# Optimization experiments

Measured on AMD Instinct MI355X. Metric: run time of the kernel, lower is better.

The kernel has to match this reference:

```python
import jax, jax.numpy as jnp
import numpy as np

N = 65536          # total detections
PER = 64           # boxes per frame (max_per_img)
B = N // PER       # frames
NUM_CLASSES = 36   # len(obj_classes), incl. background
OBJ_DIM = 192
EMB = 200
POS = 128
HID = 1024
EPS = 1e-5


def setup_inputs() -> dict:
    key = jax.random.key(0)
    ks = jax.random.split(key, 16)
    # distribution: per-box class scores over 35 foreground classes
    distribution = jax.random.uniform(ks[0], (N, NUM_CLASSES - 1), jnp.float32)
    features = jax.random.normal(ks[1], (N, OBJ_DIM), jnp.float32)
    # boxes: [img_idx, x1, y1, x2, y2], 64 boxes per frame, img_idx sorted
    img_idx = (jnp.arange(N) // PER).astype(jnp.float32)
    xy1 = jax.random.uniform(ks[2], (N, 2), jnp.float32) * 500.0
    wh = jax.random.uniform(ks[3], (N, 2), jnp.float32) * 100.0 + 1.0
    boxes = jnp.concatenate([img_idx[:, None], xy1, xy1 + wh], axis=1)
    # parameters
    obj_embed_W = jax.random.normal(ks[4], (NUM_CLASSES - 1, EMB), jnp.float32) * 0.1
    bn4_g = jnp.ones((4,), jnp.float32)
    bn4_b = jnp.zeros((4,), jnp.float32)
    bn4_m = jnp.zeros((4,), jnp.float32)
    bn4_v = jnp.ones((4,), jnp.float32)
    pos_W = jax.random.normal(ks[5], (4, POS), jnp.float32) * 0.05
    pos_b = jnp.zeros((POS,), jnp.float32)
    dec1_W = jax.random.normal(ks[6], (OBJ_DIM + EMB + POS, HID), jnp.float32) * 0.02
    dec1_b = jnp.zeros((HID,), jnp.float32)
    bn1k_g = jnp.ones((HID,), jnp.float32)
    bn1k_b = jnp.zeros((HID,), jnp.float32)
    bn1k_m = jnp.zeros((HID,), jnp.float32)
    bn1k_v = jnp.ones((HID,), jnp.float32)
    dec2_W = jax.random.normal(ks[7], (HID, NUM_CLASSES), jnp.float32) * 0.02
    dec2_b = jnp.zeros((NUM_CLASSES,), jnp.float32)
    return dict(distribution=distribution, features=features, boxes=boxes,
                obj_embed_W=obj_embed_W, bn4_g=bn4_g, bn4_b=bn4_b, bn4_m=bn4_m, bn4_v=bn4_v,
                pos_W=pos_W, pos_b=pos_b, dec1_W=dec1_W, dec1_b=dec1_b,
                bn1k_g=bn1k_g, bn1k_b=bn1k_b, bn1k_m=bn1k_m, bn1k_v=bn1k_v,
                dec2_W=dec2_W, dec2_b=dec2_b)


def reference(distribution, features, boxes, obj_embed_W, bn4_g, bn4_b, bn4_m, bn4_v,
              pos_W, pos_b, dec1_W, dec1_b, bn1k_g, bn1k_b, bn1k_m, bn1k_v,
              dec2_W, dec2_b):
    # soft object-class embedding: [N,35] @ [35,200]
    obj_embed = distribution @ obj_embed_W
    # center_size(boxes[:,1:]): (cx, cy, w, h)
    xy1 = boxes[:, 1:3]
    xy2 = boxes[:, 3:5]
    wh = xy2 - xy1 + 1.0
    cs = jnp.concatenate([xy1 + 0.5 * wh, wh], axis=1)
    # pos_embed: BatchNorm1d(4) (eval) -> Linear(4,128) -> ReLU (dropout=id in eval)
    h = (cs - bn4_m) * jax.lax.rsqrt(bn4_v + EPS) * bn4_g + bn4_b
    pos = jax.nn.relu(h @ pos_W + pos_b)
    # decoder_lin: Linear(520,1024) -> BN(1024, eval) -> ReLU -> Linear(1024,36)
    obj_feat = jnp.concatenate([features, obj_embed, pos], axis=1)  # [N,520]
    g = obj_feat @ dec1_W + dec1_b
    g = (g - bn1k_m) * jax.lax.rsqrt(bn1k_v + EPS) * bn1k_g + bn1k_b
    g = jax.nn.relu(g)
    logits = g @ dec2_W + dec2_b  # [N,36]
    # drop background, softmax over foreground classes
    dist = jax.nn.softmax(logits[:, 1:], axis=1)  # [N,35]
    pred_scores = jnp.max(dist[:, 1:], axis=1)
    pred_labels = jnp.argmax(dist[:, 1:], axis=1) + 2
    # per-frame human argmax over class-0 (human) score; 64 boxes per frame
    human_local = jnp.argmax(dist[:, 0].reshape(B, PER), axis=1)
    human_idx = jnp.arange(B) * PER + human_local  # [B]
    pred_labels = pred_labels.at[human_idx].set(1)
    pred_scores = pred_scores.at[human_idx].set(dist[human_idx, 0])
    return dist, pred_scores, pred_labels, human_idx
```

## Files before the change

### kernel.cpp

```cpp
#include <hip/hip_runtime.h>
#include <math.h>

#define NROWS 65536
#define PER 64
#define BIMG 1024
#define NCLS 36
#define OBJ_DIM 192
#define EMB 200
#define POSD 128
#define HID 1024
#define EPSV 1e-5f

#define KP 384
#define XSTR 392
#define LSTR 52


typedef __attribute__((ext_vector_type(8))) _Float16 f16x8;
typedef __attribute__((ext_vector_type(4))) _Float16 f16x4;
typedef __attribute__((ext_vector_type(4))) float f32x4;

__global__ __launch_bounds__(256) void k_fold(
    const float* __restrict__ obj_embed_W, const float* __restrict__ dec1_W,
    float* __restrict__ Fold)
{
    int e = blockIdx.x;
    int h = blockIdx.y * 256 + threadIdx.x;
    const float* A  = obj_embed_W + (size_t)e * EMB;
    const float* Bp = dec1_W + (size_t)192 * HID + h;
    float acc = 0.f;
#pragma unroll 8
    for (int j = 0; j < EMB; ++j)
        acc = fmaf(A[j], Bp[(size_t)j * HID], acc);
    Fold[(size_t)e * HID + h] = acc;
}

__global__ __launch_bounds__(256) void k_prep(
    const float* __restrict__ Fold, const float* __restrict__ dec1_W,
    const float* __restrict__ dec1_b,
    const float* __restrict__ bn1k_g, const float* __restrict__ bn1k_b,
    const float* __restrict__ bn1k_m, const float* __restrict__ bn1k_v,
    const float* __restrict__ dec2_W,
    _Float16* __restrict__ W1p, _Float16* __restrict__ W2p,
    float* __restrict__ bs)
{
    int idx = blockIdx.x * 256 + threadIdx.x;
    if (idx < HID * KP) {
        int e  = idx & 7;
        int l  = (idx >> 3) & 63;
        int ks = (idx >> 9) % 12;
        int ht = idx / 6144;
        int h = ht * 16 + (l & 15);
        int k = ks * 32 + (l >> 4) * 8 + e;
        float sc = rsqrtf(bn1k_v[h] + EPSV) * bn1k_g[h];
        float v;
        if (k < 192)      v = dec1_W[(size_t)k * HID + h];
        else if (k < 320) v = dec1_W[(size_t)(k + 200) * HID + h];
        else if (k < 355) v = Fold[(size_t)(k - 320) * HID + h];
        else              v = 0.f;
        W1p[idx] = (_Float16)(v * sc);
        if (k == 0) bs[h] = (dec1_b[h] - bn1k_m[h]) * sc + bn1k_b[h];
    } else {
        int p2 = idx - HID * KP;
        if (p2 < 64 * 3 * 256) {
            int e   = p2 & 3;
            int l   = (p2 >> 2) & 63;
            int cls = (p2 >> 8) % 3;
            int ht  = p2 / 768;
            int h = 16 * ht + 4 * (l >> 4) + e;
            int c = 16 * cls + (l & 15);
            W2p[p2] = (c < NCLS) ? (_Float16)dec2_W[(size_t)h * NCLS + c] : (_Float16)0.f;
        }
    }
}

__global__ __launch_bounds__(256, 2) void k_main(
    const float* __restrict__ distribution, const float* __restrict__ features,
    const float* __restrict__ boxes,
    const float* __restrict__ bn4_g, const float* __restrict__ bn4_b,
    const float* __restrict__ bn4_m, const float* __restrict__ bn4_v,
    const float* __restrict__ pos_W, const float* __restrict__ pos_b,
    const _Float16* __restrict__ W1p, const _Float16* __restrict__ W2p,
    const float* __restrict__ bs, const float* __restrict__ dec2_b,
    float* __restrict__ out)
{
    __shared__ __align__(16) char smem[53248];
    _Float16* Xs = (_Float16*)smem;
    float* Lst   = (float*)smem;

    int t = threadIdx.x;
    int row0 = blockIdx.x * PER;
    int wv = t >> 6, lane = t & 63, lr = lane & 15, lq = lane >> 4;

    {
        const f32x4* F4 = (const f32x4*)(features + (size_t)row0 * OBJ_DIM);
#pragma unroll
        for (int it = 0; it < 12; ++it) {
            int li = t + 256 * it;
            int r = li / 48, c4 = li % 48;
            f32x4 v = __builtin_nontemporal_load(F4 + li);
            f16x4 h4;
            h4[0] = (_Float16)v[0]; h4[1] = (_Float16)v[1];
            h4[2] = (_Float16)v[2]; h4[3] = (_Float16)v[3];
            *(f16x4*)&Xs[r * XSTR + c4 * 4] = h4;
        }
        const float* D = distribution + (size_t)row0 * (NCLS - 1);
#pragma unroll
        for (int it = 0; it < 2; ++it) {
            int li = t + 256 * it;
            int r = li >> 3, gq = li & 7;
            f16x8 v8;
#pragma unroll
            for (int e = 0; e < 8; ++e) {
                int c = gq * 8 + e;
                v8[e] = (c < 35) ? (_Float16)__builtin_nontemporal_load(D + (size_t)r * 35 + c)
                                 : (_Float16)0.f;
            }
            *(f16x8*)&Xs[r * XSTR + 320 + gq * 8] = v8;
        }
        int r = t >> 2, kq = t & 3;
        int grow = row0 + r;
        const float* bx = boxes + (size_t)grow * 5;
        float x1 = bx[1], y1 = bx[2], x2 = bx[3], y2 = bx[4];
        float w = x2 - x1 + 1.f, hh = y2 - y1 + 1.f;
        float cs[4] = {x1 + 0.5f * w, y1 + 0.5f * hh, w, hh};
        float hv[4];
#pragma unroll
        for (int i = 0; i < 4; i++)
            hv[i] = (cs[i] - bn4_m[i]) * rsqrtf(bn4_v[i] + EPSV) * bn4_g[i] + bn4_b[i];
#pragma unroll
        for (int jb = 0; jb < 4; ++jb) {
            int j0 = kq * 32 + jb * 8;
            f16x8 v8;
#pragma unroll
            for (int e = 0; e < 8; ++e) {
                int j = j0 + e;
                float p = pos_b[j];
                p = fmaf(hv[0], pos_W[j], p);
                p = fmaf(hv[1], pos_W[POSD + j], p);
                p = fmaf(hv[2], pos_W[2 * POSD + j], p);
                p = fmaf(hv[3], pos_W[3 * POSD + j], p);
                v8[e] = (_Float16)fmaxf(p, 0.f);
            }
            *(f16x8*)&Xs[r * XSTR + 192 + j0] = v8;
        }
    }
    __syncthreads();

    f32x4 Lg[4][3];
#pragma unroll
    for (int n = 0; n < 4; n++)
#pragma unroll
        for (int cls = 0; cls < 3; cls++) Lg[n][cls] = (f32x4){0.f, 0.f, 0.f, 0.f};

    for (int c0 = 0; c0 < 4; ++c0) {
        const _Float16* ap = W1p + ((size_t)(16 * c0 + wv) * 12) * 512 + (size_t)lane * 8;

        f32x4 C[4][4];
#pragma unroll
        for (int j = 0; j < 4; j++)
#pragma unroll
            for (int n = 0; n < 4; n++) C[j][n] = (f32x4){0.f, 0.f, 0.f, 0.f};

#pragma unroll 4
        for (int ks = 0; ks < 12; ++ks) {
            f16x8 ah[4], bh[4];
#pragma unroll
            for (int j = 0; j < 4; j++)
                ah[j] = *(const f16x8*)(ap + ((size_t)(4 * j) * 12 + ks) * 512);
#pragma unroll
            for (int n = 0; n < 4; n++)
                bh[n] = *(const f16x8*)&Xs[(16 * n + lr) * XSTR + ks * 32 + lq * 8];
#pragma unroll
            for (int j = 0; j < 4; j++)
#pragma unroll
                for (int n = 0; n < 4; n++)
                    C[j][n] = __builtin_amdgcn_mfma_f32_16x16x32_f16(ah[j], bh[n], C[j][n], 0, 0, 0);
        }

#pragma unroll
        for (int j = 0; j < 4; ++j) {
            int ht = 16 * c0 + wv + 4 * j;
            f32x4 bsv = *(const f32x4*)(bs + 16 * ht + 4 * lq);
            f16x4 af[4];
#pragma unroll
            for (int n = 0; n < 4; n++)
#pragma unroll
                for (int e = 0; e < 4; ++e)
                    af[n][e] = (_Float16)fmaxf(C[j][n][e] + bsv[e], 0.f);
#pragma unroll
            for (int cls = 0; cls < 3; ++cls) {
                f16x4 bf = *(const f16x4*)(W2p + ((size_t)(ht * 3 + cls) * 64 + lane) * 4);
#pragma unroll
                for (int n = 0; n < 4; n++)
                    Lg[n][cls] = __builtin_amdgcn_mfma_f32_16x16x16f16(af[n], bf, Lg[n][cls], 0, 0, 0);
            }
        }
    }

    __syncthreads();
    {
        float* Lw = Lst + (size_t)wv * 64 * LSTR;
#pragma unroll
        for (int n = 0; n < 4; n++)
#pragma unroll
            for (int cls = 0; cls < 3; cls++)
#pragma unroll
                for (int e = 0; e < 4; ++e)
                    Lw[(16 * n + 4 * lq + e) * LSTR + 16 * cls + lr] = Lg[n][cls][e];
    }
    __syncthreads();

    if (t < 64) {
        int row = row0 + t;
        float lg[36];
#pragma unroll
        for (int c = 1; c < 36; ++c)
            lg[c] = Lst[t * LSTR + c] + Lst[64 * LSTR + t * LSTR + c]
                  + Lst[128 * LSTR + t * LSTR + c] + Lst[192 * LSTR + t * LSTR + c]
                  + dec2_b[c];
        float m = lg[1];
#pragma unroll
        for (int c = 2; c < 36; ++c) m = fmaxf(m, lg[c]);
        float d[35];
        float s = 0.f;
#pragma unroll
        for (int c = 1; c < 36; ++c) { float e = expf(lg[c] - m); d[c - 1] = e; s += e; }
        float inv = 1.0f / s;
        float* dout = out + (size_t)row * 35;
#pragma unroll
        for (int j = 0; j < 35; ++j) dout[j] = d[j] * inv;

        float best = -1.f; int bi = 1;
#pragma unroll
        for (int c = 1; c < 35; ++c) {
            float v = d[c] * inv;
            if (v > best) { best = v; bi = c; }
        }

        float v0 = d[0] * inv;
        float mv = v0; int mi = t;
#pragma unroll
        for (int off = 32; off > 0; off >>= 1) {
            float ov = __shfl_down(mv, off);
            int   oi = __shfl_down(mi, off);
            if (ov > mv || (ov == mv && oi < mi)) { mv = ov; mi = oi; }
        }
        int human = __shfl(mi, 0);
        bool isH = (t == human);
        out[(size_t)NROWS * 35 + row] = isH ? v0 : best;
        out[(size_t)NROWS * 36 + row] = isH ? 1.0f : (float)(bi + 1);
        if (t == 0) out[(size_t)NROWS * 37 + blockIdx.x] = (float)(row0 + human);
    }
}

extern "C" void kernel_launch(void* const* d_in, const int* in_sizes, int n_in,
                              void* d_out, int out_size, void* d_ws, size_t ws_size,
                              hipStream_t stream)
{
    (void)in_sizes; (void)n_in; (void)out_size; (void)ws_size;
    const float* distribution = (const float*)d_in[0];
    const float* features     = (const float*)d_in[1];
    const float* boxes        = (const float*)d_in[2];
    const float* obj_embed_W  = (const float*)d_in[3];
    const float* bn4_g        = (const float*)d_in[4];
    const float* bn4_b        = (const float*)d_in[5];
    const float* bn4_m        = (const float*)d_in[6];
    const float* bn4_v        = (const float*)d_in[7];
    const float* pos_W        = (const float*)d_in[8];
    const float* pos_b        = (const float*)d_in[9];
    const float* dec1_W       = (const float*)d_in[10];
    const float* dec1_b       = (const float*)d_in[11];
    const float* bn1k_g       = (const float*)d_in[12];
    const float* bn1k_b       = (const float*)d_in[13];
    const float* bn1k_m       = (const float*)d_in[14];
    const float* bn1k_v       = (const float*)d_in[15];
    const float* dec2_W       = (const float*)d_in[16];
    const float* dec2_b       = (const float*)d_in[17];

    float* out = (float*)d_out;

    _Float16* W1p  = (_Float16*)d_ws;
    _Float16* W2p  = W1p + (size_t)HID * KP;
    float*    bsv  = (float*)(W2p + (size_t)64 * 3 * 256);
    float*    Fold = bsv + HID;

    k_fold<<<dim3(35, 4), 256, 0, stream>>>(obj_embed_W, dec1_W, Fold);

    int prep_elems = HID * KP + 64 * 3 * 256;
    k_prep<<<(prep_elems + 255) / 256, 256, 0, stream>>>(
        Fold, dec1_W, dec1_b, bn1k_g, bn1k_b, bn1k_m, bn1k_v, dec2_W,
        W1p, W2p, bsv);

    k_main<<<BIMG, 256, 0, stream>>>(
        distribution, features, boxes, bn4_g, bn4_b, bn4_m, bn4_v, pos_W, pos_b,
        W1p, W2p, bsv, dec2_b, out);
}
```

Baseline: 226.7 us.

## Process two frames per 512-thread block so wave groups share W1 slices

Each block now handles 128 rows (two frames) with 8 waves. Two groups of four waves read the same W1 tiles, each against its own 64-row half of the shared activation buffer, so weight fetches can be reused through cache. Shared memory doubles to about 104 KB and the grid halves. The ks loop unroll drops from 4 to 2. The larger LDS footprint likely limits each CU to one block, and the coarser grid may worsen tail imbalance across CUs.

```diff
diff --git a/kernel.cpp b/kernel.cpp
--- a/kernel.cpp
+++ b/kernel.cpp
@@ -4,6 +4,7 @@
 #define NROWS 65536
 #define PER 64
 #define BIMG 1024
+#define NBLK 512
 #define NCLS 36
 #define OBJ_DIM 192
 #define EMB 200
@@ -74,7 +75,7 @@
     }
 }
 
-__global__ __launch_bounds__(256, 2) void k_main(
+__global__ __launch_bounds__(512, 2) void k_main(
     const float* __restrict__ distribution, const float* __restrict__ features,
     const float* __restrict__ boxes,
     const float* __restrict__ bn4_g, const float* __restrict__ bn4_b,
@@ -84,19 +85,20 @@
     const float* __restrict__ bs, const float* __restrict__ dec2_b,
     float* __restrict__ out)
 {
-    __shared__ __align__(16) char smem[53248];
+    __shared__ __align__(16) char smem[106496];
     _Float16* Xs = (_Float16*)smem;
     float* Lst   = (float*)smem;
 
     int t = threadIdx.x;
-    int row0 = blockIdx.x * PER;
+    int row0 = blockIdx.x * 128;
     int wv = t >> 6, lane = t & 63, lr = lane & 15, lq = lane >> 4;
+    int s = wv & 3, g = wv >> 2;
 
     {
         const f32x4* F4 = (const f32x4*)(features + (size_t)row0 * OBJ_DIM);
 #pragma unroll
         for (int it = 0; it < 12; ++it) {
-            int li = t + 256 * it;
+            int li = t + 512 * it;
             int r = li / 48, c4 = li % 48;
             f32x4 v = __builtin_nontemporal_load(F4 + li);
             f16x4 h4;
@@ -107,7 +109,7 @@
         const float* D = distribution + (size_t)row0 * (NCLS - 1);
 #pragma unroll
         for (int it = 0; it < 2; ++it) {
-            int li = t + 256 * it;
+            int li = t + 512 * it;
             int r = li >> 3, gq = li & 7;
             f16x8 v8;
 #pragma unroll
@@ -154,7 +156,7 @@
         for (int cls = 0; cls < 3; cls++) Lg[n][cls] = (f32x4){0.f, 0.f, 0.f, 0.f};
 
     for (int c0 = 0; c0 < 4; ++c0) {
-        const _Float16* ap = W1p + ((size_t)(16 * c0 + wv) * 12) * 512 + (size_t)lane * 8;
+        const _Float16* ap = W1p + ((size_t)(16 * c0 + s) * 12) * 512 + (size_t)lane * 8;
 
         f32x4 C[4][4];
 #pragma unroll
@@ -162,7 +164,7 @@
 #pragma unroll
             for (int n = 0; n < 4; n++) C[j][n] = (f32x4){0.f, 0.f, 0.f, 0.f};
 
-#pragma unroll 4
+#pragma unroll 2
         for (int ks = 0; ks < 12; ++ks) {
             f16x8 ah[4], bh[4];
 #pragma unroll
@@ -170,7 +172,7 @@
                 ah[j] = *(const f16x8*)(ap + ((size_t)(4 * j) * 12 + ks) * 512);
 #pragma unroll
             for (int n = 0; n < 4; n++)
-                bh[n] = *(const f16x8*)&Xs[(16 * n + lr) * XSTR + ks * 32 + lq * 8];
+                bh[n] = *(const f16x8*)&Xs[(64 * g + 16 * n + lr) * XSTR + ks * 32 + lq * 8];
 #pragma unroll
             for (int j = 0; j < 4; j++)
 #pragma unroll
@@ -180,7 +182,7 @@
 
 #pragma unroll
         for (int j = 0; j < 4; ++j) {
-            int ht = 16 * c0 + wv + 4 * j;
+            int ht = 16 * c0 + s + 4 * j;
             f32x4 bsv = *(const f32x4*)(bs + 16 * ht + 4 * lq);
             f16x4 af[4];
 #pragma unroll
@@ -200,33 +202,34 @@
 
     __syncthreads();
     {
-        float* Lw = Lst + (size_t)wv * 64 * LSTR;
+        float* Lw = Lst + (size_t)s * 128 * LSTR;
 #pragma unroll
         for (int n = 0; n < 4; n++)
 #pragma unroll
             for (int cls = 0; cls < 3; cls++)
 #pragma unroll
                 for (int e = 0; e < 4; ++e)
-                    Lw[(16 * n + 4 * lq + e) * LSTR + 16 * cls + lr] = Lg[n][cls][e];
+                    Lw[(64 * g + 16 * n + 4 * lq + e) * LSTR + 16 * cls + lr] = Lg[n][cls][e];
     }
     __syncthreads();
 
-    if (t < 64) {
+    if (t < 128) {
+        int loc = t & 63;
         int row = row0 + t;
         float lg[36];
 #pragma unroll
         for (int c = 1; c < 36; ++c)
-            lg[c] = Lst[t * LSTR + c] + Lst[64 * LSTR + t * LSTR + c]
-                  + Lst[128 * LSTR + t * LSTR + c] + Lst[192 * LSTR + t * LSTR + c]
+            lg[c] = Lst[t * LSTR + c] + Lst[128 * LSTR + t * LSTR + c]
+                  + Lst[256 * LSTR + t * LSTR + c] + Lst[384 * LSTR + t * LSTR + c]
                   + dec2_b[c];
         float m = lg[1];
 #pragma unroll
         for (int c = 2; c < 36; ++c) m = fmaxf(m, lg[c]);
         float d[35];
-        float s = 0.f;
-#pragma unroll
-        for (int c = 1; c < 36; ++c) { float e = expf(lg[c] - m); d[c - 1] = e; s += e; }
-        float inv = 1.0f / s;
+        float s2 = 0.f;
+#pragma unroll
+        for (int c = 1; c < 36; ++c) { float e = expf(lg[c] - m); d[c - 1] = e; s2 += e; }
+        float inv = 1.0f / s2;
         float* dout = out + (size_t)row * 35;
 #pragma unroll
         for (int j = 0; j < 35; ++j) dout[j] = d[j] * inv;
@@ -239,7 +242,7 @@
         }
 
         float v0 = d[0] * inv;
-        float mv = v0; int mi = t;
+        float mv = v0; int mi = loc;
 #pragma unroll
         for (int off = 32; off > 0; off >>= 1) {
             float ov = __shfl_down(mv, off);
@@ -247,10 +250,12 @@
             if (ov > mv || (ov == mv && oi < mi)) { mv = ov; mi = oi; }
         }
         int human = __shfl(mi, 0);
-        bool isH = (t == human);
+        bool isH = (loc == human);
         out[(size_t)NROWS * 35 + row] = isH ? v0 : best;
         out[(size_t)NROWS * 36 + row] = isH ? 1.0f : (float)(bi + 1);
-        if (t == 0) out[(size_t)NROWS * 37 + blockIdx.x] = (float)(row0 + human);
+        if (loc == 0)
+            out[(size_t)NROWS * 37 + blockIdx.x * 2 + (t >> 6)]
+                = (float)(row0 + (t >> 6) * 64 + human);
     }
 }
 
@@ -292,7 +297,7 @@
         Fold, dec1_W, dec1_b, bn1k_g, bn1k_b, bn1k_m, bn1k_v, dec2_W,
         W1p, W2p, bsv);
 
-    k_main<<<BIMG, 256, 0, stream>>>(
+    k_main<<<NBLK, 512, 0, stream>>>(
         distribution, features, boxes, bn4_g, bn4_b, bn4_m, bn4_v, pos_W, pos_b,
         W1p, W2p, bsv, dec2_b, out);
 }
```

Measured after the change: 229.1 us. No clear change (+1.0%).
